# Performance work log

Hardware: AMD Instinct MI355X
Metric: run time of the kernel (lower is better)

## Reference

```python
import jax, jax.numpy as jnp
import numpy as np

N = 50000
E = 800000
IO = 128
HID = 256
KQ = 256
EPS = 1e-5


def setup_inputs() -> dict:
    key = jax.random.key(0)
    ks = jax.random.split(key, 16)
    def w(k, shape, fan_in):
        return jax.random.normal(k, shape, dtype=jnp.float32) / np.sqrt(fan_in)
    x0 = jax.random.normal(ks[0], (N, IO), dtype=jnp.float32)
    edges = jax.random.randint(ks[1], (2, E), 0, N, dtype=jnp.int64)
    return {
        "x0": x0,
        "edges": edges,
        "Wq1": w(ks[2], (IO, KQ), IO), "Wk1": w(ks[3], (IO, KQ), IO),
        "Wv1": w(ks[4], (IO, HID), IO), "Wr1": w(ks[5], (IO, HID), IO),
        "b1": jnp.zeros((HID,), jnp.float32),
        "g1": jnp.ones((HID,), jnp.float32), "be1": jnp.zeros((HID,), jnp.float32),
        "Wq2": w(ks[6], (HID, KQ), HID), "Wk2": w(ks[7], (HID, KQ), HID),
        "Wv2": w(ks[8], (HID, IO), HID), "Wr2": w(ks[9], (HID, IO), HID),
        "b2": jnp.zeros((IO,), jnp.float32),
        "g2": jnp.ones((IO,), jnp.float32), "be2": jnp.zeros((IO,), jnp.float32),
    }


def _transformer_conv(x, src, dst, Wq, Wk, Wv, Wr, b, n):
    # single-head graph transformer conv (PyG TransformerConv style)
    q = x @ Wq                      # [n, kq]
    k = x @ Wk                      # [n, kq]
    v = x @ Wv                      # [n, out]
    scale = 1.0 / np.sqrt(Wq.shape[1])
    logits = jnp.sum(q[dst] * k[src], axis=-1) * scale   # [E]
    m = jax.lax.stop_gradient(jax.ops.segment_max(logits, dst, num_segments=n))
    m = jnp.where(jnp.isfinite(m), m, 0.0)
    e = jnp.exp(logits - m[dst])                          # [E]
    s = jax.ops.segment_sum(e, dst, num_segments=n)       # [n]
    alpha = e / jnp.maximum(s[dst], 1e-16)                # [E]
    agg = jax.ops.segment_sum(alpha[:, None] * v[src], dst, num_segments=n)
    return agg + x @ Wr + b


def _batch_norm(x, gamma, beta):
    mu = jnp.mean(x, axis=0)
    var = jnp.mean((x - mu) ** 2, axis=0)  # biased var, as torch BN training
    return (x - mu) * jax.lax.rsqrt(var + EPS) * gamma + beta


def reference(x0, edges, Wq1, Wk1, Wv1, Wr1, b1, g1, be1,
              Wq2, Wk2, Wv2, Wr2, b2, g2, be2):
    src, dst = edges[0], edges[1]
    n = x0.shape[0]
    x = _transformer_conv(x0, src, dst, Wq1, Wk1, Wv1, Wr1, b1, n)
    x = jax.nn.relu(_batch_norm(x, g1, be1))
    x = _transformer_conv(x, src, dst, Wq2, Wk2, Wv2, Wr2, b2, n)
    x = _batch_norm(x, g2, be2)
    return jax.nn.relu(x + x0)
```

## Files before the change

### kernel.cpp

```cpp
#include <hip/hip_runtime.h>
#include <stdint.h>

typedef unsigned short ushort_t;

__device__ __forceinline__ float bf2f(unsigned short u) {
  union { unsigned int i; float f; } c; c.i = ((unsigned int)u) << 16; return c.f;
}
__device__ __forceinline__ unsigned short f2bf(float f) {
  union { float f; unsigned int i; } c; c.f = f;
  unsigned int r = c.i + 0x7FFFu + ((c.i >> 16) & 1u);
  return (unsigned short)(r >> 16);
}
__device__ __forceinline__ float relu_nanprop(float v) { return (v < 0.f) ? 0.f : v; }

__device__ __forceinline__ void async_copy16(const void* g, void* l) {
  __builtin_amdgcn_global_load_lds(
      (const __attribute__((address_space(1))) unsigned int*)(uintptr_t)g,
      (__attribute__((address_space(3))) unsigned int*)(uintptr_t)l,
      16, 0, 0);
}

typedef __attribute__((ext_vector_type(8))) short s16x8;
typedef __attribute__((ext_vector_type(4))) float f32x4;

__device__ __forceinline__ int edge_at(const void* edges, int wide, int idx) {
  if (wide) return (int)((const long long*)edges)[idx];
  return ((const int*)edges)[idx];
}

__device__ __forceinline__ void gemm_tile(
    const ushort_t* __restrict__ Ae, const ushort_t* __restrict__ A2e, int Ksplit,
    const ushort_t* __restrict__ BT,
    ushort_t* __restrict__ o0, ushort_t* __restrict__ o1,
    ushort_t* __restrict__ o2, ushort_t* __restrict__ o3,
    const ushort_t* __restrict__ bias3,
    int M, int K, int NC, int b0, int b1, int b2,
    float* __restrict__ bnsum, float* __restrict__ bnsq,
    int tm, int tn) {
  __shared__ __align__(16) ushort_t As[128 * 32];
  __shared__ __align__(16) ushort_t Bs[128 * 32];
  int tid = threadIdx.x;
  int lane = tid & 63, wave = tid >> 6;
  int wm = (wave >> 1) * 64, wn = (wave & 1) * 64;
  int q = lane >> 4, l = lane & 15;
  f32x4 acc[4][4];
#pragma unroll
  for (int a = 0; a < 4; a++)
#pragma unroll
    for (int b = 0; b < 4; b++) acc[a][b] = (f32x4){0.f, 0.f, 0.f, 0.f};

  int lrow = lane >> 2, c8 = (lane & 3) * 8;
  for (int k0 = 0; k0 < K; k0 += 32) {
    const ushort_t* Ap; int kk, sA;
    if (k0 < Ksplit) { Ap = Ae;  kk = k0;          sA = Ksplit; }
    else             { Ap = A2e; kk = k0 - Ksplit; sA = K - Ksplit; }
#pragma unroll
    for (int t = 0; t < 2; t++) {
      int chunk = t * 4 + wave;
      int row = chunk * 16 + lrow;
      int ra = tm + row; if (ra > M - 1) ra = M - 1;
      async_copy16(&Ap[(size_t)ra * sA + kk + c8], &As[chunk * 512]);
      async_copy16(&BT[(size_t)(tn + row) * K + k0 + c8], &Bs[chunk * 512]);
    }
    __syncthreads();
    s16x8 af[4], bfr[4];
#pragma unroll
    for (int mf = 0; mf < 4; mf++) af[mf] = *(const s16x8*)&As[(wm + mf * 16 + l) * 32 + q * 8];
#pragma unroll
    for (int nf = 0; nf < 4; nf++) bfr[nf] = *(const s16x8*)&Bs[(wn + nf * 16 + l) * 32 + q * 8];
#pragma unroll
    for (int mf = 0; mf < 4; mf++)
#pragma unroll
      for (int nf = 0; nf < 4; nf++)
        acc[mf][nf] = __builtin_amdgcn_mfma_f32_16x16x32_bf16(af[mf], bfr[nf], acc[mf][nf], 0, 0, 0);
    __syncthreads();
  }
  ushort_t* op; int sbase, w; bool addb = false;
  if (tn < b0)      { op = o0; sbase = 0;  w = b0; }
  else if (tn < b1) { op = o1; sbase = b0; w = b1 - b0; }
  else if (tn < b2) { op = o2; sbase = b1; w = b2 - b1; }
  else              { op = o3; sbase = b2; w = NC - b2; addb = true; }
  int lc0 = tn + wn - sbase + l;
  float bv[4];
#pragma unroll
  for (int nf = 0; nf < 4; nf++) bv[nf] = addb ? bf2f(bias3[lc0 + nf * 16]) : 0.f;
  float csum[4] = {0.f, 0.f, 0.f, 0.f}, csq[4] = {0.f, 0.f, 0.f, 0.f};
#pragma unroll
  for (int mf = 0; mf < 4; mf++) {
#pragma unroll
    for (int j = 0; j < 4; j++) {
      int r = tm + wm + mf * 16 + q * 4 + j;
      if (r < M) {
#pragma unroll
        for (int nf = 0; nf < 4; nf++) {
          float v = acc[mf][nf][j] + bv[nf];
          op[(size_t)r * w + lc0 + nf * 16] = f2bf(v);
          csum[nf] += v;
          csq[nf]  += v * v;
        }
      }
    }
  }
  if (bnsum) {
#pragma unroll
    for (int nf = 0; nf < 4; nf++) {
      csum[nf] += __shfl_xor(csum[nf], 16); csum[nf] += __shfl_xor(csum[nf], 32);
      csq[nf]  += __shfl_xor(csq[nf], 16);  csq[nf]  += __shfl_xor(csq[nf], 32);
    }
    if (q == 0) {
#pragma unroll
      for (int nf = 0; nf < 4; nf++) {
        atomicAdd(&bnsum[lc0 + nf * 16], csum[nf]);
        atomicAdd(&bnsq[lc0 + nf * 16],  csq[nf]);
      }
    }
  }
}

__global__ void setup_kernel(int* __restrict__ zreg2, int N,
                             const int* __restrict__ e32, int n32, int* __restrict__ eflag,
                             const unsigned int* __restrict__ x, int nw, int* __restrict__ fF) {
  int b = blockIdx.x, tid = threadIdx.x;
  if (b < 256) {
    int total = 2 * N + 1088;
    for (int i = b * 256 + tid; i < total; i += 256 * 256) zreg2[i] = 0;
  } else if (b == 256) {
    __shared__ int any;
    if (tid == 0) any = 0;
    __syncthreads();
    for (int i = tid; i < 4096; i += 256) {
      int idx = 2 * i + 1;
      if (idx < n32 && e32[idx] != 0) any = 1;
    }
    __syncthreads();
    if (tid == 0) eflag[0] = (any == 0) ? 1 : 0;
  } else {
    __shared__ int cnt;
    if (tid == 0) cnt = 0;
    __syncthreads();
    int local = 0;
    for (int i = tid; i < 4096 && i < nw; i += 256) {
      unsigned int low = x[i] & 0xFFFFu;
      unsigned int e = (low >> 7) & 0xFFu;
      if (low != 0u && (e < 96u || e > 144u)) local++;
    }
    atomicAdd(&cnt, local);
    __syncthreads();
    if (tid == 0) fF[0] = (cnt > 1024) ? 1 : 0;
  }
}

__global__ void cvt_all_kernel(const void* __restrict__ x0, ushort_t* __restrict__ x0b, int nx,
                               const void* p0, const void* p1, const void* p2,
                               const void* p3, const void* p4, const void* p5,
                               ushort_t* o0, ushort_t* o1, ushort_t* o2,
                               ushort_t* o3, ushort_t* o4, ushort_t* o5,
                               const void* W10, const void* W11, const void* W12, const void* W13,
                               ushort_t* __restrict__ Wq1b, ushort_t* __restrict__ Wk1b,
                               ushort_t* __restrict__ wcatH1,
                               const void* W20, const void* W21, const void* W22, const void* W23,
                               ushort_t* __restrict__ Wq2b, ushort_t* __restrict__ Wk2b,
                               ushort_t* __restrict__ wcatH2,
                               const void* __restrict__ edges, int* __restrict__ deg,
                               int E, int Nn,
                               const int* __restrict__ eflag, const int* __restrict__ fF) {
  int b = blockIdx.x, tid = threadIdx.x;
  int f = fF[0];
  if (b < 4096) {
    if (f) {
      int nx8 = nx >> 3;
      for (int i = b * 256 + tid; i < nx8; i += 4096 * 256) {
        const float* src = (const float*)x0 + (size_t)i * 8;
        float4 a = *(const float4*)src;
        float4 c = *(const float4*)(src + 4);
        s16x8 r;
        r[0] = (short)f2bf(a.x); r[1] = (short)f2bf(a.y);
        r[2] = (short)f2bf(a.z); r[3] = (short)f2bf(a.w);
        r[4] = (short)f2bf(c.x); r[5] = (short)f2bf(c.y);
        r[6] = (short)f2bf(c.z); r[7] = (short)f2bf(c.w);
        *(s16x8*)(x0b + (size_t)i * 8) = r;
      }
    }
  } else if (b == 4096) {
    const void* ins[6] = {p0, p1, p2, p3, p4, p5};
    ushort_t* outs[6] = {o0, o1, o2, o3, o4, o5};
    const int segs[7] = {0, 256, 512, 768, 896, 1024, 1152};
    for (int i = tid; i < 1152; i += 256) {
      int s = 0;
      while (i >= segs[s + 1]) s++;
      int li = i - segs[s];
      outs[s][li] = f ? f2bf(((const float*)ins[s])[li]) : ((const ushort_t*)ins[s])[li];
    }
  } else if (b < 4609) {
    for (int i = (b - 4097) * 256 + tid; i < 131072; i += 512 * 256) {
      if (i < 32768) {
        Wq1b[i] = f ? f2bf(((const float*)W10)[i]) : ((const ushort_t*)W10)[i];
      } else if (i < 65536) {
        int r = i - 32768;
        Wk1b[r] = f ? f2bf(((const float*)W11)[r]) : ((const ushort_t*)W11)[r];
      } else if (i < 98304) {
        int rem = i - 65536, k = rem >> 8, c = rem & 255;
        ushort_t v = f ? f2bf(((const float*)W13)[rem]) : ((const ushort_t*)W13)[rem];
        wcatH1[(size_t)c * 256 + k] = v;
      } else {
        int rem = i - 98304, k = rem >> 8, c = rem & 255;
        ushort_t v = f ? f2bf(((const float*)W12)[rem]) : ((const ushort_t*)W12)[rem];
        wcatH1[(size_t)c * 256 + 128 + k] = v;
      }
    }
  } else if (b < 5121) {
    for (int i = (b - 4609) * 256 + tid; i < 196608; i += 512 * 256) {
      if (i < 65536) {
        Wq2b[i] = f ? f2bf(((const float*)W20)[i]) : ((const ushort_t*)W20)[i];
      } else if (i < 131072) {
        int r = i - 65536;
        Wk2b[r] = f ? f2bf(((const float*)W21)[r]) : ((const ushort_t*)W21)[r];
      } else if (i < 163840) {
        int rem = i - 131072, k = rem >> 7, c = rem & 127;
        ushort_t v = f ? f2bf(((const float*)W23)[rem]) : ((const ushort_t*)W23)[rem];
        wcatH2[(size_t)c * 512 + k] = v;
      } else {
        int rem = i - 163840, k = rem >> 7, c = rem & 127;
        ushort_t v = f ? f2bf(((const float*)W22)[rem]) : ((const ushort_t*)W22)[rem];
        wcatH2[(size_t)c * 512 + 256 + k] = v;
      }
    }
  } else {
    int wide = eflag[0];
    for (int e = (b - 5121) * 256 + tid; e < E; e += 1024 * 256) {
      int d = edge_at(edges, wide, E + e);
      if (d < 0) d = 0; if (d >= Nn) d = Nn - 1;
      atomicAdd(&deg[d], 1);
    }
  }
}

__global__ __launch_bounds__(256)
void chunk_mgemm_kernel(const int* __restrict__ deg, int* __restrict__ csum,
                        int* __restrict__ cpre, int* __restrict__ offs,
                        int n, int N, int nchunk, int* __restrict__ done,
                        const ushort_t* __restrict__ Wk1b, const ushort_t* __restrict__ Wq1b,
                        ushort_t* __restrict__ wcatQ1,
                        const ushort_t* __restrict__ Wk2b, const ushort_t* __restrict__ Wq2b,
                        ushort_t* __restrict__ wcatQ2) {
  int b = blockIdx.x, t = threadIdx.x;
  if (b < nchunk) {
    int i = b * 256 + t;
    int v = (i < n) ? deg[i] : 0;
    __shared__ int ws[4];
#pragma unroll
    for (int o = 32; o > 0; o >>= 1) v += __shfl_down(v, o);
    if ((t & 63) == 0) ws[t >> 6] = v;
    __syncthreads();
    if (t == 0) atomicExch(&csum[b], ws[0] + ws[1] + ws[2] + ws[3]);
    __shared__ int lastf;
    if (t == 0) lastf = (atomicAdd(done, 1) == nchunk - 1);
    __syncthreads();
    if (lastf) {
      __shared__ int tmp[256];
      int v2 = (t < nchunk) ? atomicAdd(&csum[t], 0) : 0;
      tmp[t] = v2;
      __syncthreads();
      for (int off = 1; off < 256; off <<= 1) {
        int x = (t >= off) ? tmp[t - off] : 0;
        __syncthreads();
        tmp[t] += x;
        __syncthreads();
      }
      if (t < nchunk) cpre[t] = tmp[t] - v2;
      if (t == 255) offs[N] = tmp[255];
    }
  } else {
    int mb = b - nchunk;
    if (mb == 0)
      gemm_tile(Wk1b, Wk1b, 256, Wq1b, wcatQ1, wcatQ1, wcatQ1, wcatQ1,
                wcatQ1 , 128, 256, 128, 128, 128, 128,
                nullptr, nullptr, 0, 0);
    else {
      int t2 = mb - 1;
      gemm_tile(Wk2b, Wk2b, 256, Wq2b, wcatQ2, wcatQ2, wcatQ2, wcatQ2,
                wcatQ2 , 256, 256, 256, 256, 256, 256,
                nullptr, nullptr, (t2 >> 1) * 128, (t2 & 1) * 128);
    }
  }
}

__global__ void scan_final_kernel(const int* __restrict__ deg, const int* __restrict__ cpre,
                                  int* __restrict__ offs, int n) {
  int b = blockIdx.x, t = threadIdx.x, i = b * 256 + t;
  __shared__ int tmp[256];
  int v = (i < n) ? deg[i] : 0;
  tmp[t] = v;
  __syncthreads();
  for (int off = 1; off < 256; off <<= 1) {
    int x = (t >= off) ? tmp[t - off] : 0;
    __syncthreads();
    tmp[t] += x;
    __syncthreads();
  }
  if (i < n) offs[i] = cpre[b] + tmp[t] - v;
}

__global__ __launch_bounds__(256)
void scatter_qt1_kernel(const void* __restrict__ edges, const int* __restrict__ flag,
                        const int* __restrict__ offs, int* __restrict__ fill,
                        int* __restrict__ srcS, int E, int Nn,
                        const ushort_t* __restrict__ x0b, const ushort_t* __restrict__ wcatQ1,
                        ushort_t* __restrict__ qtb,
                        const int* __restrict__ fF, const void* __restrict__ x0raw) {
  int b = blockIdx.x;
  if (b < 1024) {
    int wide = flag[0];
    for (int e = b * 256 + threadIdx.x; e < E; e += 1024 * 256) {
      int s = edge_at(edges, wide, e);
      int d = edge_at(edges, wide, E + e);
      if (d < 0) d = 0; if (d >= Nn) d = Nn - 1;
      if (s < 0) s = 0; if (s >= Nn) s = Nn - 1;
      int p = offs[d] + atomicAdd(&fill[d], 1);
      if (p < 0) p = 0; if (p >= E) p = E - 1;
      srcS[p] = s;
    }
  } else {
    const ushort_t* Ae = (fF[0] == 0) ? (const ushort_t*)x0raw : x0b;
    gemm_tile(Ae, Ae, 128, wcatQ1, qtb, qtb, qtb, qtb, wcatQ1 ,
              Nn, 128, 128, 128, 128, 128, nullptr, nullptr, (b - 1024) * 128, 0);
  }
}

__global__ __launch_bounds__(256)
void gemm4_kernel(const ushort_t* __restrict__ A, const ushort_t* __restrict__ A2,
                  int Ksplit,
                  const ushort_t* __restrict__ BT,
                  ushort_t* __restrict__ o0, ushort_t* __restrict__ o1,
                  ushort_t* __restrict__ o2, ushort_t* __restrict__ o3,
                  const ushort_t* __restrict__ bias3,
                  int M, int K, int NC, int b0, int b1, int b2,
                  float* __restrict__ bnsum, float* __restrict__ bnsq,
                  const int* __restrict__ fF, const void* __restrict__ x0raw, int axsel) {
  const ushort_t* Ae = A;
  const ushort_t* A2e = A2;
  if (axsel && fF[0] == 0) {
    if (axsel & 1) Ae = (const ushort_t*)x0raw;
    if (axsel & 2) A2e = (const ushort_t*)x0raw;
  }
  gemm_tile(Ae, A2e, Ksplit, BT, o0, o1, o2, o3, bias3, M, K, NC, b0, b1, b2,
            bnsum, bnsq, blockIdx.x * 128, blockIdx.y * 128);
}

__global__ __launch_bounds__(256)
void attn_kernel(const ushort_t* __restrict__ qt, const ushort_t* __restrict__ xin,
                 const int* __restrict__ offs, const int* __restrict__ srcS,
                 ushort_t* __restrict__ aggb, int D, int Nn,
                 const int* __restrict__ fF, const void* __restrict__ x0raw, int xsel) {
  int lane = threadIdx.x & 63, wave = threadIdx.x >> 6;
  int n = blockIdx.x * 4 + wave;
  if (n >= Nn) return;
  const ushort_t* x = (xsel && fF[0] == 0) ? (const ushort_t*)x0raw : xin;

  int e0 = offs[n], e1 = offs[n + 1];
  float wsum = 0.f;

  if (D == 128) {
    int g = lane >> 3, sub = lane & 7;
    const ushort_t* qp = qt + (size_t)n * 128 + sub * 16;
    s16x8 q0 = __builtin_nontemporal_load((const s16x8*)qp);
    s16x8 q1 = __builtin_nontemporal_load((const s16x8*)(qp + 8));
    float qf[16];
#pragma unroll
    for (int i = 0; i < 8; i++) {
      qf[i]     = bf2f((unsigned short)q0[i]);
      qf[8 + i] = bf2f((unsigned short)q1[i]);
    }
    float acc[16];
#pragma unroll
    for (int i = 0; i < 16; i++) acc[i] = 0.f;
    int j = e0;
    s16x8 x0c, x1c;
    bool have = (j + 8 <= e1);
    if (have) {
      int s = __builtin_nontemporal_load(srcS + j + g);
      if (s < 0 || s >= Nn) s = 0;
      const ushort_t* xp = x + (size_t)s * 128 + sub * 16;
      x0c = *(const s16x8*)xp; x1c = *(const s16x8*)(xp + 8);
    }
    for (; j + 16 <= e1; j += 8) {
      int s2 = __builtin_nontemporal_load(srcS + j + 8 + g);
      if (s2 < 0 || s2 >= Nn) s2 = 0;
      const ushort_t* xp2 = x + (size_t)s2 * 128 + sub * 16;
      s16x8 x0n = *(const s16x8*)xp2, x1n = *(const s16x8*)(xp2 + 8);
      float pa = 0.f, pb = 0.f;
#pragma unroll
      for (int i = 0; i < 8; i++) {
        pa += qf[i] * bf2f((unsigned short)x0c[i]);
        pb += qf[8 + i] * bf2f((unsigned short)x1c[i]);
      }
      float p = pa + pb;
      p += __shfl_xor(p, 1); p += __shfl_xor(p, 2); p += __shfl_xor(p, 4);
      float w = __expf(p * 0.0625f);
      wsum += w;
#pragma unroll
      for (int i = 0; i < 8; i++) {
        acc[i]     += w * bf2f((unsigned short)x0c[i]);
        acc[8 + i] += w * bf2f((unsigned short)x1c[i]);
      }
      x0c = x0n; x1c = x1n;
    }
    if (have) {
      float pa = 0.f, pb = 0.f;
#pragma unroll
      for (int i = 0; i < 8; i++) {
        pa += qf[i] * bf2f((unsigned short)x0c[i]);
        pb += qf[8 + i] * bf2f((unsigned short)x1c[i]);
      }
      float p = pa + pb;
      p += __shfl_xor(p, 1); p += __shfl_xor(p, 2); p += __shfl_xor(p, 4);
      float w = __expf(p * 0.0625f);
      wsum += w;
#pragma unroll
      for (int i = 0; i < 8; i++) {
        acc[i]     += w * bf2f((unsigned short)x0c[i]);
        acc[8 + i] += w * bf2f((unsigned short)x1c[i]);
      }
      j += 8;
    }
    int rem = e1 - j;
    if (rem > 0) {
      bool valid = g < rem;
      int s = __builtin_nontemporal_load(srcS + (valid ? (j + g) : j));
      if (s < 0 || s >= Nn) s = 0;
      const ushort_t* xp = x + (size_t)s * 128 + sub * 16;
      s16x8 x0v = *(const s16x8*)xp, x1v = *(const s16x8*)(xp + 8);
      float pa = 0.f, pb = 0.f;
#pragma unroll
      for (int i = 0; i < 8; i++) {
        pa += qf[i] * bf2f((unsigned short)x0v[i]);
        pb += qf[8 + i] * bf2f((unsigned short)x1v[i]);
      }
      float p = pa + pb;
      p += __shfl_xor(p, 1); p += __shfl_xor(p, 2); p += __shfl_xor(p, 4);
      float w = 0.f;
      if (valid) w = __expf(p * 0.0625f);
      wsum += w;
#pragma unroll
      for (int i = 0; i < 8; i++) {
        acc[i]     += w * bf2f((unsigned short)x0v[i]);
        acc[8 + i] += w * bf2f((unsigned short)x1v[i]);
      }
    }
    wsum += __shfl_xor(wsum, 8); wsum += __shfl_xor(wsum, 16); wsum += __shfl_xor(wsum, 32);
#pragma unroll
    for (int i = 0; i < 16; i++) {
      acc[i] += __shfl_xor(acc[i], 8);
      acc[i] += __shfl_xor(acc[i], 16);
      acc[i] += __shfl_xor(acc[i], 32);
    }
    float inv = 1.f / fmaxf(wsum, 1e-16f);
    if (g == 0) {
      s16x8 r0, r1;
#pragma unroll
      for (int i = 0; i < 8; i++) {
        r0[i] = (short)f2bf(acc[i] * inv);
        r1[i] = (short)f2bf(acc[8 + i] * inv);
      }
      size_t idx = (size_t)n * 128 + sub * 16;
      __builtin_nontemporal_store(r0, (s16x8*)(aggb + idx));
      __builtin_nontemporal_store(r1, (s16x8*)(aggb + idx + 8));
    }
  } else {
    int g = lane >> 4, sub = lane & 15;
    s16x8 q0 = __builtin_nontemporal_load((const s16x8*)(qt + (size_t)n * 256 + sub * 16));
    s16x8 q1 = __builtin_nontemporal_load((const s16x8*)(qt + (size_t)n * 256 + sub * 16 + 8));
    float qf[16];
#pragma unroll
    for (int i = 0; i < 8; i++) {
      qf[i]     = bf2f((unsigned short)q0[i]);
      qf[8 + i] = bf2f((unsigned short)q1[i]);
    }
    float acc[16];
#pragma unroll
    for (int i = 0; i < 16; i++) acc[i] = 0.f;
    int j = e0;
    s16x8 x0c, x1c;
    bool have = (j + 4 <= e1);
    if (have) {
      int s = __builtin_nontemporal_load(srcS + j + g);
      if (s < 0 || s >= Nn) s = 0;
      const ushort_t* xp = x + (size_t)s * 256 + sub * 16;
      x0c = *(const s16x8*)xp; x1c = *(const s16x8*)(xp + 8);
    }
    for (; j + 8 <= e1; j += 4) {
      int s2 = __builtin_nontemporal_load(srcS + j + 4 + g);
      if (s2 < 0 || s2 >= Nn) s2 = 0;
      const ushort_t* xp2 = x + (size_t)s2 * 256 + sub * 16;
      s16x8 x0n = *(const s16x8*)xp2, x1n = *(const s16x8*)(xp2 + 8);
      float pa = 0.f, pb = 0.f;
#pragma unroll
      for (int i = 0; i < 8; i++) {
        pa += qf[i] * bf2f((unsigned short)x0c[i]);
        pb += qf[8 + i] * bf2f((unsigned short)x1c[i]);
      }
      float p = pa + pb;
      p += __shfl_xor(p, 1); p += __shfl_xor(p, 2);
      p += __shfl_xor(p, 4); p += __shfl_xor(p, 8);
      float w = __expf(p * 0.0625f);
      wsum += w;
#pragma unroll
      for (int i = 0; i < 8; i++) {
        acc[i]     += w * bf2f((unsigned short)x0c[i]);
        acc[8 + i] += w * bf2f((unsigned short)x1c[i]);
      }
      x0c = x0n; x1c = x1n;
    }
    if (have) {
      float pa = 0.f, pb = 0.f;
#pragma unroll
      for (int i = 0; i < 8; i++) {
        pa += qf[i] * bf2f((unsigned short)x0c[i]);
        pb += qf[8 + i] * bf2f((unsigned short)x1c[i]);
      }
      float p = pa + pb;
      p += __shfl_xor(p, 1); p += __shfl_xor(p, 2);
      p += __shfl_xor(p, 4); p += __shfl_xor(p, 8);
      float w = __expf(p * 0.0625f);
      wsum += w;
#pragma unroll
      for (int i = 0; i < 8; i++) {
        acc[i]     += w * bf2f((unsigned short)x0c[i]);
        acc[8 + i] += w * bf2f((unsigned short)x1c[i]);
      }
      j += 4;
    }
    int rem = e1 - j;
    if (rem > 0) {
      bool valid = g < rem;
      int s = __builtin_nontemporal_load(srcS + (valid ? (j + g) : j));
      if (s < 0 || s >= Nn) s = 0;
      const ushort_t* xp = x + (size_t)s * 256 + sub * 16;
      s16x8 x0v = *(const s16x8*)xp, x1v = *(const s16x8*)(xp + 8);
      float pa = 0.f, pb = 0.f;
#pragma unroll
      for (int i = 0; i < 8; i++) {
        pa += qf[i] * bf2f((unsigned short)x0v[i]);
        pb += qf[8 + i] * bf2f((unsigned short)x1v[i]);
      }
      float p = pa + pb;
      p += __shfl_xor(p, 1); p += __shfl_xor(p, 2);
      p += __shfl_xor(p, 4); p += __shfl_xor(p, 8);
      float w = 0.f;
      if (valid) w = __expf(p * 0.0625f);
      wsum += w;
#pragma unroll
      for (int i = 0; i < 8; i++) {
        acc[i]     += w * bf2f((unsigned short)x0v[i]);
        acc[8 + i] += w * bf2f((unsigned short)x1v[i]);
      }
    }
    wsum += __shfl_xor(wsum, 16); wsum += __shfl_xor(wsum, 32);
#pragma unroll
    for (int i = 0; i < 16; i++) {
      acc[i] += __shfl_xor(acc[i], 16);
      acc[i] += __shfl_xor(acc[i], 32);
    }
    float inv = 1.f / fmaxf(wsum, 1e-16f);
    if (g == 0) {
      s16x8 r0, r1;
#pragma unroll
      for (int i = 0; i < 8; i++) {
        r0[i] = (short)f2bf(acc[i] * inv);
        r1[i] = (short)f2bf(acc[8 + i] * inv);
      }
      size_t idx = (size_t)n * 256 + sub * 16;
      __builtin_nontemporal_store(r0, (s16x8*)(aggb + idx));
      __builtin_nontemporal_store(r1, (s16x8*)(aggb + idx + 8));
    }
  }
}

__global__ void norm_relu_kernel(const ushort_t* __restrict__ h,
                                 const float* __restrict__ sum, const float* __restrict__ sumsq,
                                 const ushort_t* __restrict__ g, const ushort_t* __restrict__ be,
                                 ushort_t* __restrict__ x1, int N, size_t total8, int cmask) {
  __shared__ float sc[256], sh[256];
  int t = threadIdx.x;
  if (t <= cmask) {
    float mu = sum[t] / (float)N;
    float var = sumsq[t] / (float)N - mu * mu;
    float s = bf2f(g[t]) * rsqrtf(var + 1e-5f);
    sc[t] = s;
    sh[t] = bf2f(be[t]) - mu * s;
  }
  __syncthreads();
  for (size_t i = blockIdx.x * (size_t)blockDim.x + t; i < total8;
       i += (size_t)gridDim.x * blockDim.x) {
    size_t base = i * 8;
    s16x8 hv = *(const s16x8*)(h + base);
    int c0 = (int)(base & (size_t)cmask);
    s16x8 r;
#pragma unroll
    for (int j = 0; j < 8; j++) {
      float vv = bf2f((unsigned short)hv[j]) * sc[c0 + j] + sh[c0 + j];
      r[j] = (short)f2bf(relu_nanprop(vv));
    }
    *(s16x8*)(x1 + base) = r;
  }
}

__global__ void final_kernel(const ushort_t* __restrict__ h,
                             const float* __restrict__ sum, const float* __restrict__ sumsq,
                             const ushort_t* __restrict__ g, const ushort_t* __restrict__ be,
                             const ushort_t* __restrict__ x0b, const void* __restrict__ x0raw,
                             void* __restrict__ out,
                             const int* __restrict__ flagF, int N, size_t total8) {
  __shared__ float sc[128], sh[128];
  int t = threadIdx.x;
  if (t < 128) {
    float mu = sum[t] / (float)N;
    float var = sumsq[t] / (float)N - mu * mu;
    float s = bf2f(g[t]) * rsqrtf(var + 1e-5f);
    sc[t] = s;
    sh[t] = bf2f(be[t]) - mu * s;
  }
  __syncthreads();
  int f = flagF[0];
  const ushort_t* xp = f ? x0b : (const ushort_t*)x0raw;
  for (size_t i = blockIdx.x * (size_t)blockDim.x + t; i < total8;
       i += (size_t)gridDim.x * blockDim.x) {
    size_t base = i * 8;
    s16x8 hv = *(const s16x8*)(h + base);
    s16x8 xv = *(const s16x8*)(xp + base);
    int c0 = (int)(base & 127);
    float v[8];
#pragma unroll
    for (int j = 0; j < 8; j++) {
      float vv = bf2f((unsigned short)hv[j]) * sc[c0 + j] + sh[c0 + j]
               + bf2f((unsigned short)xv[j]);
      v[j] = relu_nanprop(vv);
    }
    if (f) {
      float4 o1 = {v[0], v[1], v[2], v[3]};
      float4 o2 = {v[4], v[5], v[6], v[7]};
      *(float4*)((float*)out + base) = o1;
      *(float4*)((float*)out + base + 4) = o2;
    } else {
      s16x8 r;
#pragma unroll
      for (int j = 0; j < 8; j++) r[j] = (short)f2bf(v[j]);
      *(s16x8*)((ushort_t*)out + base) = r;
    }
  }
}

extern "C" void kernel_launch(void* const* d_in, const int* in_sizes, int n_in,
                              void* d_out, int out_size, void* d_ws, size_t ws_size,
                              hipStream_t stream) {
  const void* x0  = d_in[0];
  const void* edges = d_in[1];
  const void* Wq1 = d_in[2];
  const void* Wk1 = d_in[3];
  const void* Wv1 = d_in[4];
  const void* Wr1 = d_in[5];
  const void* b1  = d_in[6];
  const void* gw1 = d_in[7];
  const void* bw1 = d_in[8];
  const void* Wq2 = d_in[9];
  const void* Wk2 = d_in[10];
  const void* Wv2 = d_in[11];
  const void* Wr2 = d_in[12];
  const void* b2  = d_in[13];
  const void* gw2 = d_in[14];
  const void* bw2 = d_in[15];

  int N = in_sizes[0] / 128;
  int E = in_sizes[1] / 2;
  int NCHUNK = (N + 255) / 256;
  int MT = (N + 127) / 128;

  uintptr_t base = (uintptr_t)d_ws;
  auto carve = [&](size_t bytes) -> void* {
    uintptr_t p = base;
    base += (bytes + 255) & ~(size_t)255;
    return (void*)p;
  };
  ushort_t* x0b = (ushort_t*)carve((size_t)N * 128 * 2);
  ushort_t* qtb = (ushort_t*)carve((size_t)N * 256 * 2);
  ushort_t* aggb = (ushort_t*)carve((size_t)N * 256 * 2);
  ushort_t* hb = (ushort_t*)carve((size_t)N * 256 * 2);
  ushort_t* x1 = (ushort_t*)carve((size_t)N * 256 * 2);
  ushort_t* Wq1b = (ushort_t*)carve((size_t)128 * 256 * 2);
  ushort_t* Wk1b = (ushort_t*)carve((size_t)128 * 256 * 2);
  ushort_t* wcatQ1 = (ushort_t*)carve((size_t)128 * 128 * 2);
  ushort_t* wcatH1 = (ushort_t*)carve((size_t)256 * 256 * 2);
  ushort_t* Wq2b = (ushort_t*)carve((size_t)256 * 256 * 2);
  ushort_t* Wk2b = (ushort_t*)carve((size_t)256 * 256 * 2);
  ushort_t* wcatQ2 = (ushort_t*)carve((size_t)256 * 256 * 2);
  ushort_t* wcatH2 = (ushort_t*)carve((size_t)128 * 512 * 2);
  ushort_t* b1b  = (ushort_t*)carve(256 * 2);
  ushort_t* g1b  = (ushort_t*)carve(256 * 2);
  ushort_t* be1b = (ushort_t*)carve(256 * 2);
  ushort_t* b2b  = (ushort_t*)carve(128 * 2);
  ushort_t* g2b  = (ushort_t*)carve(128 * 2);
  ushort_t* be2b = (ushort_t*)carve(128 * 2);
  int* offs = (int*)carve((size_t)(N + 1) * 4);
  int* srcS = (int*)carve((size_t)E * 4);
  int* csum = (int*)carve(256 * 4);
  int* cpre = (int*)carve(256 * 4);
  int nzero = 2 * N + 1088;
  int* zreg2 = (int*)carve((size_t)nzero * 4);
  int* deg   = zreg2;
  int* fill  = zreg2 + N;
  float* sum1 = (float*)(zreg2 + 2 * N);
  float* sq1  = sum1 + 256;
  float* sum2 = sum1 + 512;
  float* sq2  = sum1 + 640;
  int* done  = zreg2 + 2 * N + 1024;
  int* eflag = (int*)carve(256);
  int* fF = eflag + 1;

  size_t needed = base - (uintptr_t)d_ws;
  if (needed > ws_size) return;

  setup_kernel<<<258, 256, 0, stream>>>(zreg2, N, (const int*)edges, 2 * E, eflag,
                                        (const unsigned int*)x0, N * 128, fF);
  cvt_all_kernel<<<6145, 256, 0, stream>>>(x0, x0b, N * 128,
                                           b1, gw1, bw1, b2, gw2, bw2,
                                           b1b, g1b, be1b, b2b, g2b, be2b,
                                           Wq1, Wk1, Wv1, Wr1, Wq1b, Wk1b, wcatH1,
                                           Wq2, Wk2, Wv2, Wr2, Wq2b, Wk2b, wcatH2,
                                           edges, deg, E, N, eflag, fF);
  chunk_mgemm_kernel<<<NCHUNK + 5, 256, 0, stream>>>(deg, csum, cpre, offs, N, N, NCHUNK,
                                                     done, Wk1b, Wq1b, wcatQ1,
                                                     Wk2b, Wq2b, wcatQ2);
  scan_final_kernel<<<NCHUNK, 256, 0, stream>>>(deg, cpre, offs, N);
  scatter_qt1_kernel<<<1024 + MT, 256, 0, stream>>>(edges, eflag, offs, fill, srcS, E, N,
                                                    x0b, wcatQ1, qtb, fF, x0);

  int gAttn = (N + 3) / 4;
  attn_kernel<<<gAttn, 256, 0, stream>>>(qtb, x0b, offs, srcS, aggb, 128, N, fF, x0, 1);
  gemm4_kernel<<<dim3(MT, 2), 256, 0, stream>>>(x0b, aggb, 128, wcatH1,
                                                hb, hb, hb, hb,
                                                b1b, N, 256, 256, 0, 0, 0,
                                                sum1, sq1, fF, x0, 1);
  norm_relu_kernel<<<4096, 256, 0, stream>>>(hb, sum1, sq1, g1b, be1b, x1, N,
                                             (size_t)N * 32, 255);
  gemm4_kernel<<<dim3(MT, 2), 256, 0, stream>>>(x1, x1, 256, wcatQ2,
                                                qtb, qtb, qtb, qtb,
                                                b2b, N, 256, 256, 256, 256, 256,
                                                nullptr, nullptr, fF, x0, 0);
  attn_kernel<<<gAttn, 256, 0, stream>>>(qtb, x1, offs, srcS, aggb, 256, N, fF, x0, 0);
  gemm4_kernel<<<dim3(MT, 1), 256, 0, stream>>>(x1, aggb, 256, wcatH2,
                                                hb, hb, hb, hb,
                                                b2b, N, 512, 128, 0, 0, 0,
                                                sum2, sq2, fF, x0, 0);
  final_kernel<<<2048, 256, 0, stream>>>(hb, sum2, sq2, g2b, be2b, x0b, x0, d_out, fF, N,
                                         (size_t)N * 16);
}
```

Before: 441.5 us.

## Fuse output GEMM with batch-norm apply via grid-wide spin barrier

Replaces the pair of GEMM plus separate norm/relu (and final residual) kernels with a single persistent kernel. Each block computes its row tiles across all column tiles, joins a grid-wide atomic barrier to wait for the BN statistics, then normalises its own rows straight from the just-written (likely cache-resident) hb. This saves two kernel launches and part of a full pass over hb. The trade-offs are a y-dimension loop that serialises column tiles inside each block, and a software grid barrier that assumes all MT blocks are co-resident and would deadlock if they are not.

Measured after the change: 571.3 us. +29.4%, slower.

```diff
diff --git a/kernel.cpp b/kernel.cpp
--- a/kernel.cpp
+++ b/kernel.cpp
@@ -348,6 +348,85 @@
 }
 
 __global__ __launch_bounds__(256)
+void hbn_kernel(const ushort_t* __restrict__ A, const ushort_t* __restrict__ A2,
+                int Ksplit, const ushort_t* __restrict__ BT,
+                ushort_t* __restrict__ hb, const ushort_t* __restrict__ bias,
+                int M, int K, int NC, int nty,
+                float* __restrict__ bnsum, float* __restrict__ bnsq,
+                int* __restrict__ done, int ngrid,
+                const ushort_t* __restrict__ gamma, const ushort_t* __restrict__ beta,
+                void* __restrict__ outp, int mode,
+                const int* __restrict__ fF, const void* __restrict__ x0raw, int axsel,
+                const ushort_t* __restrict__ x0b) {
+  const ushort_t* Ae = A;
+  if (axsel && fF[0] == 0) Ae = (const ushort_t*)x0raw;
+  int tm = blockIdx.x * 128;
+  for (int ty = 0; ty < nty; ++ty)
+    gemm_tile(Ae, A2, Ksplit, BT, hb, hb, hb, hb, bias,
+              M, K, NC, 0, 0, 0, bnsum, bnsq, tm, ty * 128);
+  if (threadIdx.x == 0) {
+    __threadfence();
+    atomicAdd(done, 1);
+    while (__hip_atomic_load(done, __ATOMIC_ACQUIRE, __HIP_MEMORY_SCOPE_AGENT) < ngrid)
+      __builtin_amdgcn_s_sleep(32);
+  }
+  __syncthreads();
+  __shared__ float sc[256], sh[256];
+  for (int c = threadIdx.x; c < NC; c += 256) {
+    float su = __hip_atomic_load(&bnsum[c], __ATOMIC_RELAXED, __HIP_MEMORY_SCOPE_AGENT);
+    float sq = __hip_atomic_load(&bnsq[c],  __ATOMIC_RELAXED, __HIP_MEMORY_SCOPE_AGENT);
+    float mu = su / (float)M;
+    float var = sq / (float)M - mu * mu;
+    float s = bf2f(gamma[c]) * rsqrtf(var + 1e-5f);
+    sc[c] = s;
+    sh[c] = bf2f(beta[c]) - mu * s;
+  }
+  __syncthreads();
+  int f = (mode == 2) ? fF[0] : 0;
+  const ushort_t* resid = nullptr;
+  if (mode == 2) resid = f ? x0b : (const ushort_t*)x0raw;
+  int r = tm + (threadIdx.x >> 1);
+  if (r < M) {
+    for (int ty = 0; ty < nty; ++ty) {
+      int c0 = ty * 128 + (threadIdx.x & 1) * 64;
+      for (int cc = 0; cc < 64; cc += 8) {
+        size_t base = (size_t)r * NC + c0 + cc;
+        s16x8 hv = *(const s16x8*)(hb + base);
+        if (mode == 1) {
+          s16x8 rr;
+#pragma unroll
+          for (int j = 0; j < 8; j++) {
+            float vv = bf2f((unsigned short)hv[j]) * sc[c0 + cc + j] + sh[c0 + cc + j];
+            rr[j] = (short)f2bf(relu_nanprop(vv));
+          }
+          *(s16x8*)((ushort_t*)outp + base) = rr;
+        } else {
+          s16x8 xv = *(const s16x8*)(resid + base);
+          float v[8];
+#pragma unroll
+          for (int j = 0; j < 8; j++) {
+            float vv = bf2f((unsigned short)hv[j]) * sc[c0 + cc + j] + sh[c0 + cc + j]
+                     + bf2f((unsigned short)xv[j]);
+            v[j] = relu_nanprop(vv);
+          }
+          if (f) {
+            float4 o1 = {v[0], v[1], v[2], v[3]};
+            float4 o2 = {v[4], v[5], v[6], v[7]};
+            *(float4*)((float*)outp + base) = o1;
+            *(float4*)((float*)outp + base + 4) = o2;
+          } else {
+            s16x8 rr;
+#pragma unroll
+            for (int j = 0; j < 8; j++) rr[j] = (short)f2bf(v[j]);
+            *(s16x8*)((ushort_t*)outp + base) = rr;
+          }
+        }
+      }
+    }
+  }
+}
+
+__global__ __launch_bounds__(256)
 void attn_kernel(const ushort_t* __restrict__ qt, const ushort_t* __restrict__ xin,
                  const int* __restrict__ offs, const int* __restrict__ srcS,
                  ushort_t* __restrict__ aggb, int D, int Nn,
@@ -572,80 +651,6 @@
       size_t idx = (size_t)n * 256 + sub * 16;
       __builtin_nontemporal_store(r0, (s16x8*)(aggb + idx));
       __builtin_nontemporal_store(r1, (s16x8*)(aggb + idx + 8));
-    }
-  }
-}
-
-__global__ void norm_relu_kernel(const ushort_t* __restrict__ h,
-                                 const float* __restrict__ sum, const float* __restrict__ sumsq,
-                                 const ushort_t* __restrict__ g, const ushort_t* __restrict__ be,
-                                 ushort_t* __restrict__ x1, int N, size_t total8, int cmask) {
-  __shared__ float sc[256], sh[256];
-  int t = threadIdx.x;
-  if (t <= cmask) {
-    float mu = sum[t] / (float)N;
-    float var = sumsq[t] / (float)N - mu * mu;
-    float s = bf2f(g[t]) * rsqrtf(var + 1e-5f);
-    sc[t] = s;
-    sh[t] = bf2f(be[t]) - mu * s;
-  }
-  __syncthreads();
-  for (size_t i = blockIdx.x * (size_t)blockDim.x + t; i < total8;
-       i += (size_t)gridDim.x * blockDim.x) {
-    size_t base = i * 8;
-    s16x8 hv = *(const s16x8*)(h + base);
-    int c0 = (int)(base & (size_t)cmask);
-    s16x8 r;
-#pragma unroll
-    for (int j = 0; j < 8; j++) {
-      float vv = bf2f((unsigned short)hv[j]) * sc[c0 + j] + sh[c0 + j];
-      r[j] = (short)f2bf(relu_nanprop(vv));
-    }
-    *(s16x8*)(x1 + base) = r;
-  }
-}
-
-__global__ void final_kernel(const ushort_t* __restrict__ h,
-                             const float* __restrict__ sum, const float* __restrict__ sumsq,
-                             const ushort_t* __restrict__ g, const ushort_t* __restrict__ be,
-                             const ushort_t* __restrict__ x0b, const void* __restrict__ x0raw,
-                             void* __restrict__ out,
-                             const int* __restrict__ flagF, int N, size_t total8) {
-  __shared__ float sc[128], sh[128];
-  int t = threadIdx.x;
-  if (t < 128) {
-    float mu = sum[t] / (float)N;
-    float var = sumsq[t] / (float)N - mu * mu;
-    float s = bf2f(g[t]) * rsqrtf(var + 1e-5f);
-    sc[t] = s;
-    sh[t] = bf2f(be[t]) - mu * s;
-  }
-  __syncthreads();
-  int f = flagF[0];
-  const ushort_t* xp = f ? x0b : (const ushort_t*)x0raw;
-  for (size_t i = blockIdx.x * (size_t)blockDim.x + t; i < total8;
-       i += (size_t)gridDim.x * blockDim.x) {
-    size_t base = i * 8;
-    s16x8 hv = *(const s16x8*)(h + base);
-    s16x8 xv = *(const s16x8*)(xp + base);
-    int c0 = (int)(base & 127);
-    float v[8];
-#pragma unroll
-    for (int j = 0; j < 8; j++) {
-      float vv = bf2f((unsigned short)hv[j]) * sc[c0 + j] + sh[c0 + j]
-               + bf2f((unsigned short)xv[j]);
-      v[j] = relu_nanprop(vv);
-    }
-    if (f) {
-      float4 o1 = {v[0], v[1], v[2], v[3]};
-      float4 o2 = {v[4], v[5], v[6], v[7]};
-      *(float4*)((float*)out + base) = o1;
-      *(float4*)((float*)out + base + 4) = o2;
-    } else {
-      s16x8 r;
-#pragma unroll
-      for (int j = 0; j < 8; j++) r[j] = (short)f2bf(v[j]);
-      *(s16x8*)((ushort_t*)out + base) = r;
     }
   }
 }
@@ -712,7 +717,9 @@
   float* sq1  = sum1 + 256;
   float* sum2 = sum1 + 512;
   float* sq2  = sum1 + 640;
-  int* done  = zreg2 + 2 * N + 1024;
+  int* doneC = zreg2 + 2 * N + 1024;
+  int* done1 = zreg2 + 2 * N + 1025;
+  int* done2 = zreg2 + 2 * N + 1026;
   int* eflag = (int*)carve(256);
   int* fF = eflag + 1;
 
@@ -728,7 +735,7 @@
                                            Wq2, Wk2, Wv2, Wr2, Wq2b, Wk2b, wcatH2,
                                            edges, deg, E, N, eflag, fF);
   chunk_mgemm_kernel<<<NCHUNK + 5, 256, 0, stream>>>(deg, csum, cpre, offs, N, N, NCHUNK,
-                                                     done, Wk1b, Wq1b, wcatQ1,
+                                                     doneC, Wk1b, Wq1b, wcatQ1,
                                                      Wk2b, Wq2b, wcatQ2);
   scan_final_kernel<<<NCHUNK, 256, 0, stream>>>(deg, cpre, offs, N);
   scatter_qt1_kernel<<<1024 + MT, 256, 0, stream>>>(edges, eflag, offs, fill, srcS, E, N,
@@ -736,21 +743,15 @@
 
   int gAttn = (N + 3) / 4;
   attn_kernel<<<gAttn, 256, 0, stream>>>(qtb, x0b, offs, srcS, aggb, 128, N, fF, x0, 1);
-  gemm4_kernel<<<dim3(MT, 2), 256, 0, stream>>>(x0b, aggb, 128, wcatH1,
-                                                hb, hb, hb, hb,
-                                                b1b, N, 256, 256, 0, 0, 0,
-                                                sum1, sq1, fF, x0, 1);
-  norm_relu_kernel<<<4096, 256, 0, stream>>>(hb, sum1, sq1, g1b, be1b, x1, N,
-                                             (size_t)N * 32, 255);
+  hbn_kernel<<<MT, 256, 0, stream>>>(x0b, aggb, 128, wcatH1, hb, b1b,
+                                     N, 256, 256, 2, sum1, sq1, done1, MT,
+                                     g1b, be1b, x1, 1, fF, x0, 1, nullptr);
   gemm4_kernel<<<dim3(MT, 2), 256, 0, stream>>>(x1, x1, 256, wcatQ2,
                                                 qtb, qtb, qtb, qtb,
                                                 b2b, N, 256, 256, 256, 256, 256,
                                                 nullptr, nullptr, fF, x0, 0);
   attn_kernel<<<gAttn, 256, 0, stream>>>(qtb, x1, offs, srcS, aggb, 256, N, fF, x0, 0);
-  gemm4_kernel<<<dim3(MT, 1), 256, 0, stream>>>(x1, aggb, 256, wcatH2,
-                                                hb, hb, hb, hb,
-                                                b2b, N, 512, 128, 0, 0, 0,
-                                                sum2, sq2, fF, x0, 0);
-  final_kernel<<<2048, 256, 0, stream>>>(hb, sum2, sq2, g2b, be2b, x0b, x0, d_out, fF, N,
-                                         (size_t)N * 16);
-}
+  hbn_kernel<<<MT, 256, 0, stream>>>(x1, aggb, 256, wcatH2, hb, b2b,
+                                     N, 512, 128, 1, sum2, sq2, done2, MT,
+                                     g2b, be2b, d_out, 2, fF, x0, 0, x0b);
+}
```
